# Optimization experiments

Measured on AMD Instinct MI355X. Metric: run time of the kernel, lower is better.

Reference implementation:

```python
import jax, jax.numpy as jnp
import numpy as np

MASK_VALUE = -1e10  # matches module's -10000000000.0


def setup_inputs() -> dict:
    key = jax.random.key(0)
    k1, k2, k3, k4, k5 = jax.random.split(key, 5)
    B, NQ, NKV, D = 32, 32, 8, 128
    NUM_PAGES, TPP, PAGES_PER_SLOT = 4096, 16, 128
    query = jax.random.normal(k1, (B, 1, NQ, D), dtype=jnp.float32)
    key_pages = jax.random.normal(k2, (NKV, NUM_PAGES, TPP, D), dtype=jnp.float32)
    value_pages = jax.random.normal(k3, (NKV, NUM_PAGES, TPP, D), dtype=jnp.float32)
    page_map = jax.random.randint(k4, (B, PAGES_PER_SLOT), 0, NUM_PAGES, dtype=jnp.int32)
    seq_lengths = jax.random.randint(k5, (B,), 1, PAGES_PER_SLOT * TPP + 1, dtype=jnp.int32)
    return {
        "query": query,
        "key_pages": key_pages,
        "value_pages": value_pages,
        "page_map": page_map,
        "seq_lengths": seq_lengths,
    }


def reference(query, key_pages, value_pages, page_map, seq_lengths):
    """Paged attention, decode mode (single query token per sequence, GQA).

    query:       [B, 1, NQ, D]
    key_pages:   [NKV, NUM_PAGES, TPP, D]
    value_pages: [NKV, NUM_PAGES, TPP, D]
    page_map:    [B, P] page indices per sequence
    seq_lengths: [B] valid kv tokens per sequence
    """
    B, _, NQ, D = query.shape
    NKV, _, TPP, _ = key_pages.shape
    G = NQ // NKV  # GQA group size
    # take last query position -> [B, NKV, G, D]
    q = query[:, -1].reshape(B, NKV, G, D)
    # gather pages per sequence: [NKV, B, P, TPP, D] -> [B, NKV, S, D]
    k = jnp.moveaxis(key_pages[:, page_map], 0, 1).reshape(B, NKV, -1, D)
    v = jnp.moveaxis(value_pages[:, page_map], 0, 1).reshape(B, NKV, -1, D)
    S = k.shape[2]
    scores = jnp.einsum("bkgd,bksd->bkgs", q, k)  # [B, NKV, G, S]
    valid = jnp.arange(S)[None, :] < seq_lengths[:, None]  # [B, S]
    scores = jnp.where(valid[:, None, None, :], scores, MASK_VALUE)
    weights = jax.nn.softmax(scores, axis=-1)
    out = jnp.einsum("bkgs,bksd->bkgd", weights, v)  # [B, NKV, G, D]
    return out.reshape(B, 1, NQ, D)
```

## Files before the change

kernel.cpp:

```cpp
#include <hip/hip_runtime.h>
#include <math.h>

#define NB      32
#define NKV     8
#define NQ      32
#define GQ      4
#define DH      128
#define TPP     16
#define PPS     128
#define NPAGES  4096
#define NSPLIT  8
#define NBK     (NB*NKV)
#define PAGE_F  (TPP*DH)
#define PART_F  (GQ*DH + 2*GQ)

__global__ __launch_bounds__(256) void pa_partial(
    const float* __restrict__ query,
    const float* __restrict__ key_pages,
    const float* __restrict__ value_pages,
    const int*   __restrict__ page_map,
    const int*   __restrict__ seq_lengths,
    float*       __restrict__ ws)
{
    const int blk = blockIdx.x;
    const int sp  = blk >> 8;
    const int bk  = blk & (NBK - 1);
    const int kv  = bk & (NKV - 1);
    const int b   = bk >> 3;
    const int tid = threadIdx.x;

    const int seq     = seq_lengths[b];
    const int n_pages = (seq + TPP - 1) / TPP;
    if (sp >= n_pages) return;

    __shared__ __align__(16) float kbuf[TPP * DH];
    __shared__ __align__(16) float vbuf[TPP * DH];
    __shared__ float s_sc[GQ][TPP];

    const int lane = tid & 63;
    const int wv   = tid >> 6;
    const int tok  = wv * 4 + (lane >> 4);
    const int l16  = lane & 15;
    const int d0   = l16 * 8;

    const int d  = tid & 127;
    const int gA = tid >> 7;
    const int gB = gA + 2;

    float qreg[GQ][8];
    #pragma unroll
    for (int g = 0; g < GQ; ++g) {
        const float4* qp = (const float4*)(query + (size_t)((b * NQ + kv * GQ + g) * DH + d0));
        const float4 a = qp[0], c = qp[1];
        qreg[g][0] = a.x; qreg[g][1] = a.y; qreg[g][2] = a.z; qreg[g][3] = a.w;
        qreg[g][4] = c.x; qreg[g][5] = c.y; qreg[g][6] = c.z; qreg[g][7] = c.w;
    }

    float mA = -INFINITY, mB = -INFINITY;
    float lA = 0.f, lB = 0.f;
    float accA = 0.f, accB = 0.f;

    for (int p = sp; p < n_pages; p += NSPLIT) {
        const int pg = page_map[b * PPS + p];
        const float4* kg = (const float4*)(key_pages   + (size_t)(kv * NPAGES + pg) * PAGE_F);
        const float4* vg = (const float4*)(value_pages + (size_t)(kv * NPAGES + pg) * PAGE_F);

        __syncthreads();
        {
            float4* kb = (float4*)kbuf;
            float4* vb = (float4*)vbuf;
            kb[tid]       = kg[tid];
            kb[tid + 256] = kg[tid + 256];
            vb[tid]       = vg[tid];
            vb[tid + 256] = vg[tid + 256];
        }
        __syncthreads();

        float part0, part1, part2, part3;
        {
            const float4 k0 = *(const float4*)&kbuf[tok * DH + d0];
            const float4 k1 = *(const float4*)&kbuf[tok * DH + d0 + 4];
            part0 = qreg[0][0]*k0.x + qreg[0][1]*k0.y + qreg[0][2]*k0.z + qreg[0][3]*k0.w
                  + qreg[0][4]*k1.x + qreg[0][5]*k1.y + qreg[0][6]*k1.z + qreg[0][7]*k1.w;
            part1 = qreg[1][0]*k0.x + qreg[1][1]*k0.y + qreg[1][2]*k0.z + qreg[1][3]*k0.w
                  + qreg[1][4]*k1.x + qreg[1][5]*k1.y + qreg[1][6]*k1.z + qreg[1][7]*k1.w;
            part2 = qreg[2][0]*k0.x + qreg[2][1]*k0.y + qreg[2][2]*k0.z + qreg[2][3]*k0.w
                  + qreg[2][4]*k1.x + qreg[2][5]*k1.y + qreg[2][6]*k1.z + qreg[2][7]*k1.w;
            part3 = qreg[3][0]*k0.x + qreg[3][1]*k0.y + qreg[3][2]*k0.z + qreg[3][3]*k0.w
                  + qreg[3][4]*k1.x + qreg[3][5]*k1.y + qreg[3][6]*k1.z + qreg[3][7]*k1.w;
            #pragma unroll
            for (int off = 8; off >= 1; off >>= 1) {
                part0 += __shfl_xor(part0, off);
                part1 += __shfl_xor(part1, off);
                part2 += __shfl_xor(part2, off);
                part3 += __shfl_xor(part3, off);
            }
        }
        const int tglob = p * TPP + tok;
        if (l16 < GQ) {
            const float val = (l16 == 0) ? part0 : (l16 == 1) ? part1
                            : (l16 == 2) ? part2 : part3;
            s_sc[l16][tok] = (tglob < seq) ? val : -1e30f;
        }
        __syncthreads();

        float sA[TPP], sB[TPP];
        #pragma unroll
        for (int t = 0; t < TPP; ++t) { sA[t] = s_sc[gA][t]; sB[t] = s_sc[gB][t]; }

        float pA = -1e30f, pB = -1e30f;
        #pragma unroll
        for (int t = 0; t < TPP; ++t) { pA = fmaxf(pA, sA[t]); pB = fmaxf(pB, sB[t]); }

        const float mnA = fmaxf(mA, pA), mnB = fmaxf(mB, pB);
        const float scA = __expf(mA - mnA), scB = __expf(mB - mnB);
        mA = mnA; mB = mnB;

        float sumA = 0.f, sumB = 0.f;
        #pragma unroll
        for (int t = 0; t < TPP; ++t) {
            sA[t] = __expf(sA[t] - mnA); sumA += sA[t];
            sB[t] = __expf(sB[t] - mnB); sumB += sB[t];
        }
        lA = lA * scA + sumA;
        lB = lB * scB + sumB;
        accA *= scA;
        accB *= scB;

        #pragma unroll
        for (int t = 0; t < TPP; ++t) {
            const float v = vbuf[t * DH + d];
            accA += sA[t] * v;
            accB += sB[t] * v;
        }
    }

    float* base = ws + (size_t)(bk * NSPLIT + sp) * PART_F;
    base[gA * DH + d] = accA;
    base[gB * DH + d] = accB;
    if (d == 0) {
        base[GQ * DH + gA]      = mA;
        base[GQ * DH + GQ + gA] = lA;
        base[GQ * DH + gB]      = mB;
        base[GQ * DH + GQ + gB] = lB;
    }
}

__global__ __launch_bounds__(256) void pa_combine(
    const float* __restrict__ ws,
    const int*   __restrict__ seq_lengths,
    float*       __restrict__ out)
{
    const int blk = blockIdx.x;
    const int b   = blk >> 3;
    const int kv  = blk & 7;
    const int tid = threadIdx.x;
    const int d   = tid & 127;
    const int gA  = tid >> 7;
    const int gB  = gA + 2;

    const int seq     = seq_lengths[b];
    const int n_pages = (seq + TPP - 1) / TPP;
    const int ns      = (n_pages < NSPLIT) ? n_pages : NSPLIT;

    const float* base0 = ws + (size_t)blk * NSPLIT * PART_F;

    float MA = -INFINITY, MB = -INFINITY;
    for (int si = 0; si < ns; ++si) {
        const float* p = base0 + si * PART_F;
        MA = fmaxf(MA, p[GQ * DH + gA]);
        MB = fmaxf(MB, p[GQ * DH + gB]);
    }

    float LA = 0.f, LB = 0.f, oA = 0.f, oB = 0.f;
    for (int si = 0; si < ns; ++si) {
        const float* p = base0 + si * PART_F;
        const float eA = __expf(p[GQ * DH + gA] - MA);
        const float eB = __expf(p[GQ * DH + gB] - MB);
        LA += p[GQ * DH + GQ + gA] * eA;
        LB += p[GQ * DH + GQ + gB] * eB;
        oA += p[gA * DH + d] * eA;
        oB += p[gB * DH + d] * eB;
    }

    float* ob = out + (size_t)(b * NQ + kv * GQ) * DH;
    ob[gA * DH + d] = oA / LA;
    ob[gB * DH + d] = oB / LB;
}

extern "C" void kernel_launch(void* const* d_in, const int* in_sizes, int n_in,
                              void* d_out, int out_size, void* d_ws, size_t ws_size,
                              hipStream_t stream)
{
    const float* query       = (const float*)d_in[0];
    const float* key_pages   = (const float*)d_in[1];
    const float* value_pages = (const float*)d_in[2];
    const int*   page_map    = (const int*)d_in[3];
    const int*   seq_lengths = (const int*)d_in[4];
    float*       out         = (float*)d_out;
    float*       ws          = (float*)d_ws;

    pa_partial<<<NSPLIT * NBK, 256, 0, stream>>>(
        query, key_pages, value_pages, page_map, seq_lengths, ws);
    pa_combine<<<NBK, 256, 0, stream>>>(ws, seq_lengths, out);
}
```

Baseline: 64.40 us.

## Double the split count and register-prefetch the next KV page

The split count rises from 8 to 16, giving more blocks per sequence. Block indexing changes so that the splits of one (batch, head) pair sit next to each other. The K/V page for the next iteration is now loaded into registers while the current page is being processed, so global loads overlap with compute. In exchange, register pressure goes up and the combine step has more partials to merge.

Result: faster. 61.04 us (-5.2%).

```diff
diff --git a/kernel.cpp b/kernel.cpp
--- a/kernel.cpp
+++ b/kernel.cpp
@@ -9,7 +9,7 @@
 #define TPP     16
 #define PPS     128
 #define NPAGES  4096
-#define NSPLIT  8
+#define NSPLIT  16
 #define NBK     (NB*NKV)
 #define PAGE_F  (TPP*DH)
 #define PART_F  (GQ*DH + 2*GQ)
@@ -23,8 +23,8 @@
     float*       __restrict__ ws)
 {
     const int blk = blockIdx.x;
-    const int sp  = blk >> 8;
-    const int bk  = blk & (NBK - 1);
+    const int sp  = blk & (NSPLIT - 1);
+    const int bk  = blk / NSPLIT;
     const int kv  = bk & (NKV - 1);
     const int b   = bk >> 3;
     const int tid = threadIdx.x;
@@ -56,23 +56,39 @@
         qreg[g][4] = c.x; qreg[g][5] = c.y; qreg[g][6] = c.z; qreg[g][7] = c.w;
     }
 
+    const float4* kbase = (const float4*)(key_pages   + (size_t)kv * NPAGES * PAGE_F);
+    const float4* vbase = (const float4*)(value_pages + (size_t)kv * NPAGES * PAGE_F);
+
     float mA = -INFINITY, mB = -INFINITY;
     float lA = 0.f, lB = 0.f;
     float accA = 0.f, accB = 0.f;
 
+    float4 rk0, rk1, rv0, rv1;
+    {
+        const int pg = page_map[b * PPS + sp];
+        const float4* kg = kbase + (size_t)pg * (PAGE_F / 4);
+        const float4* vg = vbase + (size_t)pg * (PAGE_F / 4);
+        rk0 = kg[tid]; rk1 = kg[tid + 256];
+        rv0 = vg[tid]; rv1 = vg[tid + 256];
+    }
+
     for (int p = sp; p < n_pages; p += NSPLIT) {
-        const int pg = page_map[b * PPS + p];
-        const float4* kg = (const float4*)(key_pages   + (size_t)(kv * NPAGES + pg) * PAGE_F);
-        const float4* vg = (const float4*)(value_pages + (size_t)(kv * NPAGES + pg) * PAGE_F);
-
         __syncthreads();
         {
             float4* kb = (float4*)kbuf;
             float4* vb = (float4*)vbuf;
-            kb[tid]       = kg[tid];
-            kb[tid + 256] = kg[tid + 256];
-            vb[tid]       = vg[tid];
-            vb[tid + 256] = vg[tid + 256];
+            kb[tid]       = rk0;
+            kb[tid + 256] = rk1;
+            vb[tid]       = rv0;
+            vb[tid + 256] = rv1;
+        }
+        const int pn = p + NSPLIT;
+        if (pn < n_pages) {
+            const int pg = page_map[b * PPS + pn];
+            const float4* kg = kbase + (size_t)pg * (PAGE_F / 4);
+            const float4* vg = vbase + (size_t)pg * (PAGE_F / 4);
+            rk0 = kg[tid]; rk1 = kg[tid + 256];
+            rv0 = vg[tid]; rv1 = vg[tid + 256];
         }
         __syncthreads();
 
@@ -200,7 +216,7 @@
     float*       out         = (float*)d_out;
     float*       ws          = (float*)d_ws;
 
-    pa_partial<<<NSPLIT * NBK, 256, 0, stream>>>(
+    pa_partial<<<NBK * NSPLIT, 256, 0, stream>>>(
         query, key_pages, value_pages, page_map, seq_lengths, ws);
     pa_combine<<<NBK, 256, 0, stream>>>(ws, seq_lengths, out);
 }
```

## Register-resident per-token online softmax with page prefetch and more splits

Applied to the files above, without the earlier changes.

Drops the shared-memory staging of each K/V page. Each 16-thread group now owns one token and keeps its K/V slice in registers, running an online softmax per token and prefetching the next page's K/V while computing the current one. Per-group partial results are merged through shared memory once at the end of the block. The split count rises from 8 to 16 and the block index mapping changes to interleave splits. This removes the per-page barriers and LDS traffic and adds memory-level parallelism, at the cost of more registers, a larger shared-memory merge, and more partials for the combine kernel to read.

Measured after the change: 58.04 us. -9.9%, faster.

```diff
diff --git a/kernel.cpp b/kernel.cpp
--- a/kernel.cpp
+++ b/kernel.cpp
@@ -9,7 +9,7 @@
 #define TPP     16
 #define PPS     128
 #define NPAGES  4096
-#define NSPLIT  8
+#define NSPLIT  16
 #define NBK     (NB*NKV)
 #define PAGE_F  (TPP*DH)
 #define PART_F  (GQ*DH + 2*GQ)
@@ -23,8 +23,8 @@
     float*       __restrict__ ws)
 {
     const int blk = blockIdx.x;
-    const int sp  = blk >> 8;
-    const int bk  = blk & (NBK - 1);
+    const int sp  = blk & (NSPLIT - 1);
+    const int bk  = blk >> 4;
     const int kv  = bk & (NKV - 1);
     const int b   = bk >> 3;
     const int tid = threadIdx.x;
@@ -33,19 +33,9 @@
     const int n_pages = (seq + TPP - 1) / TPP;
     if (sp >= n_pages) return;
 
-    __shared__ __align__(16) float kbuf[TPP * DH];
-    __shared__ __align__(16) float vbuf[TPP * DH];
-    __shared__ float s_sc[GQ][TPP];
-
-    const int lane = tid & 63;
-    const int wv   = tid >> 6;
-    const int tok  = wv * 4 + (lane >> 4);
-    const int l16  = lane & 15;
-    const int d0   = l16 * 8;
-
-    const int d  = tid & 127;
-    const int gA = tid >> 7;
-    const int gB = gA + 2;
+    const int grp = tid >> 4;
+    const int l16 = tid & 15;
+    const int d0  = l16 * 8;
 
     float qreg[GQ][8];
     #pragma unroll
@@ -56,93 +46,108 @@
         qreg[g][4] = c.x; qreg[g][5] = c.y; qreg[g][6] = c.z; qreg[g][7] = c.w;
     }
 
-    float mA = -INFINITY, mB = -INFINITY;
-    float lA = 0.f, lB = 0.f;
-    float accA = 0.f, accB = 0.f;
+    const float* kbase = key_pages   + (size_t)kv * NPAGES * PAGE_F;
+    const float* vbase = value_pages + (size_t)kv * NPAGES * PAGE_F;
+    const int*   pmap  = page_map + b * PPS;
+
+    float m[GQ] = {-1e30f, -1e30f, -1e30f, -1e30f};
+    float l[GQ] = {0.f, 0.f, 0.f, 0.f};
+    float acc[GQ][8] = {};
+
+    float4 ck0, ck1, cv0, cv1;
+    {
+        const size_t po = (size_t)pmap[sp] * PAGE_F + grp * DH + d0;
+        const float4* kp = (const float4*)(kbase + po);
+        const float4* vp = (const float4*)(vbase + po);
+        ck0 = kp[0]; ck1 = kp[1];
+        cv0 = vp[0]; cv1 = vp[1];
+    }
 
     for (int p = sp; p < n_pages; p += NSPLIT) {
-        const int pg = page_map[b * PPS + p];
-        const float4* kg = (const float4*)(key_pages   + (size_t)(kv * NPAGES + pg) * PAGE_F);
-        const float4* vg = (const float4*)(value_pages + (size_t)(kv * NPAGES + pg) * PAGE_F);
-
-        __syncthreads();
-        {
-            float4* kb = (float4*)kbuf;
-            float4* vb = (float4*)vbuf;
-            kb[tid]       = kg[tid];
-            kb[tid + 256] = kg[tid + 256];
-            vb[tid]       = vg[tid];
-            vb[tid + 256] = vg[tid + 256];
+        float4 nk0, nk1, nv0, nv1;
+        const int pn = p + NSPLIT;
+        if (pn < n_pages) {
+            const size_t po = (size_t)pmap[pn] * PAGE_F + grp * DH + d0;
+            const float4* kp = (const float4*)(kbase + po);
+            const float4* vp = (const float4*)(vbase + po);
+            nk0 = kp[0]; nk1 = kp[1];
+            nv0 = vp[0]; nv1 = vp[1];
         }
-        __syncthreads();
-
-        float part0, part1, part2, part3;
-        {
-            const float4 k0 = *(const float4*)&kbuf[tok * DH + d0];
-            const float4 k1 = *(const float4*)&kbuf[tok * DH + d0 + 4];
-            part0 = qreg[0][0]*k0.x + qreg[0][1]*k0.y + qreg[0][2]*k0.z + qreg[0][3]*k0.w
-                  + qreg[0][4]*k1.x + qreg[0][5]*k1.y + qreg[0][6]*k1.z + qreg[0][7]*k1.w;
-            part1 = qreg[1][0]*k0.x + qreg[1][1]*k0.y + qreg[1][2]*k0.z + qreg[1][3]*k0.w
-                  + qreg[1][4]*k1.x + qreg[1][5]*k1.y + qreg[1][6]*k1.z + qreg[1][7]*k1.w;
-            part2 = qreg[2][0]*k0.x + qreg[2][1]*k0.y + qreg[2][2]*k0.z + qreg[2][3]*k0.w
-                  + qreg[2][4]*k1.x + qreg[2][5]*k1.y + qreg[2][6]*k1.z + qreg[2][7]*k1.w;
-            part3 = qreg[3][0]*k0.x + qreg[3][1]*k0.y + qreg[3][2]*k0.z + qreg[3][3]*k0.w
-                  + qreg[3][4]*k1.x + qreg[3][5]*k1.y + qreg[3][6]*k1.z + qreg[3][7]*k1.w;
+
+        const float kx[8] = {ck0.x, ck0.y, ck0.z, ck0.w, ck1.x, ck1.y, ck1.z, ck1.w};
+        float s[GQ];
+        #pragma unroll
+        for (int g = 0; g < GQ; ++g) {
+            float t = qreg[g][0]*kx[0] + qreg[g][1]*kx[1] + qreg[g][2]*kx[2] + qreg[g][3]*kx[3]
+                    + qreg[g][4]*kx[4] + qreg[g][5]*kx[5] + qreg[g][6]*kx[6] + qreg[g][7]*kx[7];
             #pragma unroll
-            for (int off = 8; off >= 1; off >>= 1) {
-                part0 += __shfl_xor(part0, off);
-                part1 += __shfl_xor(part1, off);
-                part2 += __shfl_xor(part2, off);
-                part3 += __shfl_xor(part3, off);
-            }
+            for (int off = 8; off >= 1; off >>= 1) t += __shfl_xor(t, off);
+            s[g] = t;
         }
-        const int tglob = p * TPP + tok;
-        if (l16 < GQ) {
-            const float val = (l16 == 0) ? part0 : (l16 == 1) ? part1
-                            : (l16 == 2) ? part2 : part3;
-            s_sc[l16][tok] = (tglob < seq) ? val : -1e30f;
+
+        const bool valid = (p * TPP + grp) < seq;
+        const float vx[8] = {cv0.x, cv0.y, cv0.z, cv0.w, cv1.x, cv1.y, cv1.z, cv1.w};
+
+        #pragma unroll
+        for (int g = 0; g < GQ; ++g) {
+            const float mn = fmaxf(m[g], s[g]);
+            float pc = __expf(s[g] - mn);
+            pc = valid ? pc : 0.f;
+            const float sc = __expf(m[g] - mn);
+            m[g] = mn;
+            l[g] = l[g] * sc + pc;
+            #pragma unroll
+            for (int j = 0; j < 8; ++j)
+                acc[g][j] = acc[g][j] * sc + pc * vx[j];
         }
-        __syncthreads();
-
-        float sA[TPP], sB[TPP];
+
+        ck0 = nk0; ck1 = nk1; cv0 = nv0; cv1 = nv1;
+    }
+
+    __shared__ float s_acc[16][GQ][DH];
+    __shared__ float s_m[16][GQ];
+    __shared__ float s_l[16][GQ];
+
+    #pragma unroll
+    for (int g = 0; g < GQ; ++g) {
+        *(float4*)&s_acc[grp][g][d0]     = make_float4(acc[g][0], acc[g][1], acc[g][2], acc[g][3]);
+        *(float4*)&s_acc[grp][g][d0 + 4] = make_float4(acc[g][4], acc[g][5], acc[g][6], acc[g][7]);
+    }
+    if (l16 == 0) {
         #pragma unroll
-        for (int t = 0; t < TPP; ++t) { sA[t] = s_sc[gA][t]; sB[t] = s_sc[gB][t]; }
-
-        float pA = -1e30f, pB = -1e30f;
-        #pragma unroll
-        for (int t = 0; t < TPP; ++t) { pA = fmaxf(pA, sA[t]); pB = fmaxf(pB, sB[t]); }
-
-        const float mnA = fmaxf(mA, pA), mnB = fmaxf(mB, pB);
-        const float scA = __expf(mA - mnA), scB = __expf(mB - mnB);
-        mA = mnA; mB = mnB;
-
-        float sumA = 0.f, sumB = 0.f;
-        #pragma unroll
-        for (int t = 0; t < TPP; ++t) {
-            sA[t] = __expf(sA[t] - mnA); sumA += sA[t];
-            sB[t] = __expf(sB[t] - mnB); sumB += sB[t];
-        }
-        lA = lA * scA + sumA;
-        lB = lB * scB + sumB;
-        accA *= scA;
-        accB *= scB;
-
-        #pragma unroll
-        for (int t = 0; t < TPP; ++t) {
-            const float v = vbuf[t * DH + d];
-            accA += sA[t] * v;
-            accB += sB[t] * v;
-        }
+        for (int g = 0; g < GQ; ++g) { s_m[grp][g] = m[g]; s_l[grp][g] = l[g]; }
+    }
+    __syncthreads();
+
+    const int d  = tid & 127;
+    const int gA = tid >> 7;
+    const int gB = gA + 2;
+
+    float MA = -1e30f, MB = -1e30f;
+    #pragma unroll
+    for (int i = 0; i < 16; ++i) {
+        MA = fmaxf(MA, s_m[i][gA]);
+        MB = fmaxf(MB, s_m[i][gB]);
+    }
+    float LA = 0.f, LB = 0.f, oA = 0.f, oB = 0.f;
+    #pragma unroll
+    for (int i = 0; i < 16; ++i) {
+        const float eA = __expf(s_m[i][gA] - MA);
+        const float eB = __expf(s_m[i][gB] - MB);
+        LA += s_l[i][gA] * eA;
+        LB += s_l[i][gB] * eB;
+        oA += s_acc[i][gA][d] * eA;
+        oB += s_acc[i][gB][d] * eB;
     }
 
     float* base = ws + (size_t)(bk * NSPLIT + sp) * PART_F;
-    base[gA * DH + d] = accA;
-    base[gB * DH + d] = accB;
+    base[gA * DH + d] = oA;
+    base[gB * DH + d] = oB;
     if (d == 0) {
-        base[GQ * DH + gA]      = mA;
-        base[GQ * DH + GQ + gA] = lA;
-        base[GQ * DH + gB]      = mB;
-        base[GQ * DH + GQ + gB] = lB;
+        base[GQ * DH + gA]      = MA;
+        base[GQ * DH + GQ + gA] = LA;
+        base[GQ * DH + gB]      = MB;
+        base[GQ * DH + GQ + gB] = LB;
     }
 }
 
@@ -165,7 +170,7 @@
 
     const float* base0 = ws + (size_t)blk * NSPLIT * PART_F;
 
-    float MA = -INFINITY, MB = -INFINITY;
+    float MA = -1e30f, MB = -1e30f;
     for (int si = 0; si < ns; ++si) {
         const float* p = base0 + si * PART_F;
         MA = fmaxf(MA, p[GQ * DH + gA]);
@@ -200,7 +205,7 @@
     float*       out         = (float*)d_out;
     float*       ws          = (float*)d_ws;
 
-    pa_partial<<<NSPLIT * NBK, 256, 0, stream>>>(
+    pa_partial<<<NBK * NSPLIT, 256, 0, stream>>>(
         query, key_pages, value_pages, page_map, seq_lengths, ws);
     pa_combine<<<NBK, 256, 0, stream>>>(ws, seq_lengths, out);
 }
```
